# Kernel optimization log

Measured on AMD Instinct MI355X. Metric: run time of the kernel, lower is better.

Reference implementation:

```python
import jax, jax.numpy as jnp
import numpy as np
import math

B, L, H, D, HID = 2, 1024, 16, 64, 1024  # batch, seq, heads, head_dim, hidden_size


def _rope_tables(seq_len, dim):
    inv_freq = 1.0 / (10000.0 ** (jnp.arange(0, dim, 2, dtype=jnp.float32) / dim))
    t = jnp.arange(seq_len, dtype=jnp.float32)
    freqs = jnp.outer(t, inv_freq)            # (L, D/2)
    emb = jnp.concatenate([freqs, freqs], -1)  # (L, D)
    return jnp.cos(emb), jnp.sin(emb)


def _rotate_half(x):
    x1, x2 = jnp.split(x, 2, axis=-1)
    return jnp.concatenate([-x2, x1], axis=-1)


def _apply_rope(x, cos, sin):
    # x: (B,H,L,D); cos/sin: (1,1,L,D)
    return x * cos + _rotate_half(x) * sin


def setup_inputs() -> dict:
    key = jax.random.key(0)
    ks = jax.random.split(key, 8)
    s = 0.02
    return {
        "x": jax.random.normal(ks[0], (B, L, HID), jnp.float32),
        "w_qkv": jax.random.normal(ks[1], (HID, 3 * H * D), jnp.float32) * s,
        "w_o": jax.random.normal(ks[2], (H * D, HID), jnp.float32) * s,
        "log_p": jax.random.normal(ks[3], (H, 1, 1), jnp.float32) * 0.02,
        "log_a": jax.random.normal(ks[4], (H, 1, 1), jnp.float32) * 0.02,
        "w1": jax.random.normal(ks[5], (2 * H, 2 * H), jnp.float32) * s,
        "b1": jnp.zeros((2 * H,), jnp.float32),
        "w2": jax.random.normal(ks[6], (2 * H, H), jnp.float32) * s,
        "b2": jnp.zeros((H,), jnp.float32),
    }


def _forward(x, w_qkv, w_o, log_p, log_a, w1, b1, w2, b2):
    Bx, Lx, _ = x.shape
    qkv = jnp.dot(x, w_qkv).reshape(Bx, Lx, 3, H, D)
    qkv = jnp.transpose(qkv, (2, 0, 3, 1, 4))  # (3,B,H,L,D)
    q, k, v = qkv[0], qkv[1], qkv[2]

    cos, sin = _rope_tables(Lx, D)
    cos, sin = cos[None, None], sin[None, None]
    q = _apply_rope(q, cos, sin)
    k = _apply_rope(k, cos, sin)

    scale = 1.0 / math.sqrt(D)
    scores = jnp.einsum('bhid,bhjd->bhij', q, k) * scale  # (B,H,L,L)

    # Kerple bias: -p * log1p(a * |m-n|), per head
    pos = jnp.arange(Lx, dtype=jnp.float32)
    dist = jnp.abs(pos[None, :] - pos[:, None])            # (L,L)
    p = jax.nn.softplus(log_p)
    a = jax.nn.softplus(log_a)
    kerple = -p * jnp.log1p(a * dist[None])                # (H,L,L)

    # DAPE MLP refinement over head channel
    attn_t = jnp.transpose(scores, (0, 2, 3, 1))           # (B,L,L,H)
    kerple_t = jnp.broadcast_to(jnp.transpose(kerple, (1, 2, 0))[None], attn_t.shape)
    combined = jnp.concatenate([attn_t, kerple_t], axis=-1)  # (B,L,L,2H)
    hdn = jax.nn.gelu(jnp.dot(combined, w1) + b1, approximate=False)
    refined = jnp.dot(hdn, w2) + b2                        # (B,L,L,H)
    refined = jnp.transpose(refined, (0, 3, 1, 2))         # (B,H,L,L)

    scores = scores + kerple[None] + refined

    causal = jnp.tril(jnp.ones((Lx, Lx), dtype=bool))
    scores = jnp.where(causal[None, None], scores, -jnp.inf)
    weights = jax.nn.softmax(scores, axis=-1)
    out = jnp.einsum('bhij,bhjd->bhid', weights, v)        # (B,H,L,D)
    out = jnp.transpose(out, (0, 2, 1, 3)).reshape(Bx, Lx, H * D)
    return jnp.dot(out, w_o)


def reference(x, w_qkv, w_o, log_p, log_a, w1, b1, w2, b2):
    return _forward(x, w_qkv, w_o, log_p, log_a, w1, b1, w2, b2)
```

## Files before the change

kernel.cpp:

```cpp
#include <hip/hip_runtime.h>
#include <math.h>

#define Bv 2
#define Lv 1024
#define Hv 16
#define Dv 64
#define HIDv 1024

typedef unsigned short u16;
typedef short bf16x8 __attribute__((ext_vector_type(8)));
typedef unsigned short u16x4 __attribute__((ext_vector_type(4)));
typedef float f32x4 __attribute__((ext_vector_type(4)));

__device__ __forceinline__ u16 f2b(float f) {
    union { float f; unsigned u; } v; v.f = f;
    return (u16)((v.u + 0x8000u) >> 16);
}
__device__ __forceinline__ float b2f(u16 h) {
    union { unsigned u; float f; } v; v.u = ((unsigned)h) << 16;
    return v.f;
}

__device__ __forceinline__ void gl2lds16(const u16* g, u16* l) {
    __builtin_amdgcn_global_load_lds(
        (const __attribute__((address_space(1))) unsigned int*)g,
        (__attribute__((address_space(3))) unsigned int*)l,
        16, 0, 0);
}

__device__ __forceinline__ float gelu_fast(float x) {
    float x2 = x * x;
    float inner = __builtin_fmaf(0.044715f * x2, x, x);
    float e = __expf(-1.5957691216057308f * inner);
    return x / (1.0f + e);
}

__global__ __launch_bounds__(256) void qkv_rope(
    const u16* __restrict__ A, const u16* __restrict__ B,
    const float* __restrict__ ctab, const float* __restrict__ stab,
    u16* __restrict__ q, u16* __restrict__ k, u16* __restrict__ vT)
{
    __shared__ u16 As[128 * 32];
    __shared__ u16 Bs[128 * 32];
    __shared__ u16 Ct[128 * 136];

    const int m0 = blockIdx.y * 128;
    const int n0 = blockIdx.x * 128;
    const int K = 1024;

    const int tid = threadIdx.x;
    const int lane = tid & 63;
    const int wave = tid >> 6;
    const int wm0 = (wave >> 1) * 64;
    const int wn0 = (wave & 1) * 64;
    const int fr = lane & 15;
    const int fq = lane >> 4;

    f32x4 acc[4][4];
    #pragma unroll
    for (int i = 0; i < 4; ++i)
        #pragma unroll
        for (int j = 0; j < 4; ++j) acc[i][j] = (f32x4){0.f, 0.f, 0.f, 0.f};

    for (int k0 = 0; k0 < K; k0 += 32) {
        #pragma unroll
        for (int it = 0; it < 2; ++it) {
            int cid = tid + it * 256;
            int r = cid >> 2, ch = cid & 3;
            gl2lds16(A + (long long)(m0 + r) * K + k0 + ch * 8, &As[cid * 8]);
        }
        #pragma unroll
        for (int it = 0; it < 2; ++it) {
            int cid = tid + it * 256;
            int r = cid >> 2, ch = cid & 3;
            gl2lds16(B + (long long)(n0 + r) * K + k0 + ch * 8, &Bs[cid * 8]);
        }
        __syncthreads();
        bf16x8 af[4], bfr[4];
        #pragma unroll
        for (int i = 0; i < 4; ++i)
            af[i] = *(const bf16x8*)&As[(wm0 + i * 16 + fr) * 32 + fq * 8];
        #pragma unroll
        for (int j = 0; j < 4; ++j)
            bfr[j] = *(const bf16x8*)&Bs[(wn0 + j * 16 + fr) * 32 + fq * 8];
        #pragma unroll
        for (int i = 0; i < 4; ++i)
            #pragma unroll
            for (int j = 0; j < 4; ++j)
                acc[i][j] = __builtin_amdgcn_mfma_f32_16x16x32_bf16(
                    af[i], bfr[j], acc[i][j], 0, 0, 0);
        __syncthreads();
    }

    const int b = m0 >> 10;

    if (n0 >= 2048) {
        #pragma unroll
        for (int i = 0; i < 4; ++i)
            #pragma unroll
            for (int j = 0; j < 4; ++j) {
                int vcol = (n0 - 2048) + wn0 + j * 16 + fr;
                int head = vcol >> 6, d = vcol & 63;
                int l = ((m0 + wm0 + i * 16 + fq * 4) & 1023);
                u16 o[4];
                #pragma unroll
                for (int r = 0; r < 4; ++r) o[r] = f2b(acc[i][j][r]);
                *(u16x4*)&vT[((long long)(b * 16 + head) * 64 + d) * 1024 + l] =
                    *(u16x4*)o;
            }
        return;
    }

    #pragma unroll
    for (int i = 0; i < 4; ++i)
        #pragma unroll
        for (int j = 0; j < 4; ++j)
            #pragma unroll
            for (int r = 0; r < 4; ++r)
                Ct[(wm0 + i * 16 + fq * 4 + r) * 136 + wn0 + j * 16 + fr] =
                    f2b(acc[i][j][r]);
    __syncthreads();

    u16* dst = (n0 >= 1024) ? k : q;
    const int nh = n0 & 1023;
    #pragma unroll
    for (int c = 0; c < 8; ++c) {
        int cid = tid + c * 256;
        int row = cid >> 4, kc = cid & 15;
        int l = (m0 + row) & 1023;
        int head = (nh >> 6) + (kc >> 3);
        int d0 = (kc & 7) * 8;
        bf16x8 x  = *(const bf16x8*)&Ct[row * 136 + kc * 8];
        bf16x8 xp = *(const bf16x8*)&Ct[row * 136 + (kc ^ 4) * 8];
        float4 c0 = *(const float4*)&ctab[l * 64 + d0];
        float4 c1 = *(const float4*)&ctab[l * 64 + d0 + 4];
        float4 s0 = *(const float4*)&stab[l * 64 + d0];
        float4 s1 = *(const float4*)&stab[l * 64 + d0 + 4];
        float ct[8] = {c0.x, c0.y, c0.z, c0.w, c1.x, c1.y, c1.z, c1.w};
        float st[8] = {s0.x, s0.y, s0.z, s0.w, s1.x, s1.y, s1.z, s1.w};
        u16 o[8];
        #pragma unroll
        for (int e = 0; e < 8; ++e)
            o[e] = f2b(b2f((u16)x[e]) * ct[e] + b2f((u16)xp[e]) * st[e]);
        *(bf16x8*)&dst[((long long)(b * 16 + head) * 1024 + l) * 64 + d0] =
            *(bf16x8*)o;
    }
}

template<int BM, int BN, int WM, int WN, bool CBF16>
__global__ __launch_bounds__(256) void gemm_bt(
    const u16* __restrict__ A, const u16* __restrict__ B, void* __restrict__ Cv,
    int M, int N, int K, float alpha)
{
    constexpr int NW = BN / WN;
    constexpr int MI = WM / 16;
    constexpr int NI = WN / 16;
    constexpr int LDB = BN + 8;
    constexpr int LDF = BN + 4;
    __shared__ u16 As[BM * 32];
    __shared__ u16 Bs[BN * 32];
    __shared__ u16 Ctb[CBF16 ? BM * LDB : 1];
    __shared__ float Ctf[CBF16 ? 1 : BM * LDF];

    const int m0 = blockIdx.y * BM;
    const int n0 = blockIdx.x * BN;

    const int tid = threadIdx.x;
    const int lane = tid & 63;
    const int wave = tid >> 6;
    const int wm0 = (wave / NW) * WM;
    const int wn0 = (wave % NW) * WN;
    const int fr = lane & 15;
    const int fq = lane >> 4;

    f32x4 acc[MI][NI];
    #pragma unroll
    for (int i = 0; i < MI; ++i)
        #pragma unroll
        for (int j = 0; j < NI; ++j) acc[i][j] = (f32x4){0.f, 0.f, 0.f, 0.f};

    for (int k0 = 0; k0 < K; k0 += 32) {
        #pragma unroll
        for (int it = 0; it < BM / 64; ++it) {
            int cid = tid + it * 256;
            int r = cid >> 2, ch = cid & 3;
            gl2lds16(A + (long long)(m0 + r) * K + k0 + ch * 8, &As[cid * 8]);
        }
        #pragma unroll
        for (int it = 0; it < BN / 64; ++it) {
            int cid = tid + it * 256;
            int r = cid >> 2, ch = cid & 3;
            gl2lds16(B + (long long)(n0 + r) * K + k0 + ch * 8, &Bs[cid * 8]);
        }
        __syncthreads();
        bf16x8 af[MI], bfr[NI];
        #pragma unroll
        for (int i = 0; i < MI; ++i)
            af[i] = *(const bf16x8*)&As[(wm0 + i * 16 + fr) * 32 + fq * 8];
        #pragma unroll
        for (int j = 0; j < NI; ++j)
            bfr[j] = *(const bf16x8*)&Bs[(wn0 + j * 16 + fr) * 32 + fq * 8];
        #pragma unroll
        for (int i = 0; i < MI; ++i)
            #pragma unroll
            for (int j = 0; j < NI; ++j)
                acc[i][j] = __builtin_amdgcn_mfma_f32_16x16x32_bf16(
                    af[i], bfr[j], acc[i][j], 0, 0, 0);
        __syncthreads();
    }

    #pragma unroll
    for (int i = 0; i < MI; ++i)
        #pragma unroll
        for (int j = 0; j < NI; ++j)
            #pragma unroll
            for (int r = 0; r < 4; ++r) {
                int row = wm0 + i * 16 + fq * 4 + r;
                int col = wn0 + j * 16 + fr;
                float v = acc[i][j][r] * alpha;
                if (CBF16) Ctb[row * LDB + col] = f2b(v);
                else       Ctf[row * LDF + col] = v;
            }
    __syncthreads();
    if (CBF16) {
        constexpr int CPR = BN / 8;
        #pragma unroll
        for (int c = 0; c < (BM * BN) / (8 * 256); ++c) {
            int cid = tid + c * 256;
            int row = cid / CPR, kc = cid % CPR;
            *(bf16x8*)((u16*)Cv + (long long)(m0 + row) * N + n0 + kc * 8) =
                *(const bf16x8*)&Ctb[row * LDB + kc * 8];
        }
    } else {
        constexpr int CPR = BN / 4;
        #pragma unroll
        for (int c = 0; c < (BM * BN) / (4 * 256); ++c) {
            int cid = tid + c * 256;
            int row = cid / CPR, kc = cid % CPR;
            *(float4*)((float*)Cv + (long long)(m0 + row) * N + n0 + kc * 4) =
                *(const float4*)&Ctf[row * LDF + kc * 4];
        }
    }
}

__global__ __launch_bounds__(256) void qk_direct(
    const u16* __restrict__ Q, const u16* __restrict__ K, u16* __restrict__ S)
{
    const int m0 = blockIdx.y * 128;
    const int n0 = blockIdx.x * 128;
    if (n0 > m0) return;
    const u16* A = Q + (long long)blockIdx.z * 65536;
    const u16* B = K + (long long)blockIdx.z * 65536;
    u16* C = S + (long long)blockIdx.z * 1048576;

    __shared__ u16 Ct[128 * 136];

    const int tid = threadIdx.x;
    const int lane = tid & 63;
    const int wave = tid >> 6;
    const int wm0 = (wave >> 1) * 64;
    const int wn0 = (wave & 1) * 64;
    const int fr = lane & 15;
    const int fq = lane >> 4;

    bf16x8 af[4][2], bfr[4][2];
    #pragma unroll
    for (int i = 0; i < 4; ++i)
        #pragma unroll
        for (int p = 0; p < 2; ++p) {
            af[i][p]  = *(const bf16x8*)&A[(m0 + wm0 + i * 16 + fr) * 64 + p * 32 + fq * 8];
            bfr[i][p] = *(const bf16x8*)&B[(n0 + wn0 + i * 16 + fr) * 64 + p * 32 + fq * 8];
        }

    f32x4 acc[4][4];
    #pragma unroll
    for (int i = 0; i < 4; ++i)
        #pragma unroll
        for (int j = 0; j < 4; ++j) acc[i][j] = (f32x4){0.f, 0.f, 0.f, 0.f};

    #pragma unroll
    for (int p = 0; p < 2; ++p)
        #pragma unroll
        for (int i = 0; i < 4; ++i)
            #pragma unroll
            for (int j = 0; j < 4; ++j)
                acc[i][j] = __builtin_amdgcn_mfma_f32_16x16x32_bf16(
                    af[i][p], bfr[j][p], acc[i][j], 0, 0, 0);

    #pragma unroll
    for (int i = 0; i < 4; ++i)
        #pragma unroll
        for (int j = 0; j < 4; ++j)
            #pragma unroll
            for (int r = 0; r < 4; ++r)
                Ct[(wm0 + i * 16 + fq * 4 + r) * 136 + wn0 + j * 16 + fr] =
                    f2b(acc[i][j][r] * 0.125f);
    __syncthreads();
    #pragma unroll
    for (int c = 0; c < 8; ++c) {
        int cid = tid + c * 256;
        int row = cid >> 4, kc = cid & 15;
        *(bf16x8*)&C[(long long)(m0 + row) * 1024 + n0 + kc * 8] =
            *(const bf16x8*)&Ct[row * 136 + kc * 8];
    }
}

__global__ __launch_bounds__(256) void pv_direct(
    const u16* __restrict__ W, const u16* __restrict__ VT, u16* __restrict__ O)
{
    const int m0 = blockIdx.x * 64;
    const int bh = blockIdx.y;
    const u16* A = W + (long long)bh * 1048576;
    const u16* B = VT + (long long)bh * 65536;
    const int b = bh >> 4, h = bh & 15;

    __shared__ u16 Ct[64 * 72];

    const int tid = threadIdx.x;
    const int lane = tid & 63;
    const int wave = tid >> 6;
    const int wm0 = (wave >> 1) * 32;
    const int wn0 = (wave & 1) * 32;
    const int fr = lane & 15;
    const int fq = lane >> 4;

    f32x4 acc[2][2];
    #pragma unroll
    for (int i = 0; i < 2; ++i)
        #pragma unroll
        for (int j = 0; j < 2; ++j) acc[i][j] = (f32x4){0.f, 0.f, 0.f, 0.f};

    const int Kend = m0 + 64;
    for (int k0 = 0; k0 < Kend; k0 += 64) {
        bf16x8 af[2][2], bfr[2][2];
        #pragma unroll
        for (int p = 0; p < 2; ++p) {
            #pragma unroll
            for (int i = 0; i < 2; ++i)
                af[p][i] = *(const bf16x8*)&A[(m0 + wm0 + i * 16 + fr) * 1024 + k0 + p * 32 + fq * 8];
            #pragma unroll
            for (int j = 0; j < 2; ++j)
                bfr[p][j] = *(const bf16x8*)&B[(wn0 + j * 16 + fr) * 1024 + k0 + p * 32 + fq * 8];
        }
        #pragma unroll
        for (int p = 0; p < 2; ++p)
            #pragma unroll
            for (int i = 0; i < 2; ++i)
                #pragma unroll
                for (int j = 0; j < 2; ++j)
                    acc[i][j] = __builtin_amdgcn_mfma_f32_16x16x32_bf16(
                        af[p][i], bfr[p][j], acc[i][j], 0, 0, 0);
    }

    #pragma unroll
    for (int i = 0; i < 2; ++i)
        #pragma unroll
        for (int j = 0; j < 2; ++j)
            #pragma unroll
            for (int r = 0; r < 4; ++r)
                Ct[(wm0 + i * 16 + fq * 4 + r) * 72 + wn0 + j * 16 + fr] =
                    f2b(acc[i][j][r]);
    __syncthreads();
    const long long ob = (long long)b * 1048576 + h * 64;
    #pragma unroll
    for (int c = 0; c < 2; ++c) {
        int cid = tid + c * 256;
        int row = cid >> 3, kc = cid & 7;
        *(bf16x8*)&O[ob + (long long)(m0 + row) * 1024 + kc * 8] =
            *(const bf16x8*)&Ct[row * 72 + kc * 8];
    }
}

__global__ __launch_bounds__(256) void prep(
    const float* __restrict__ x, u16* __restrict__ x_bf,
    const float* __restrict__ w_qkv, u16* __restrict__ wqkvT,
    const float* __restrict__ w_o, u16* __restrict__ woT,
    const float* __restrict__ log_p, const float* __restrict__ log_a,
    u16* __restrict__ ktab, float* __restrict__ ctab, float* __restrict__ stab)
{
    __shared__ float tile[64][65];
    const int bid = blockIdx.x;
    const int tid = threadIdx.x;

    if (bid < 8192) {
        int i = bid * 256 + tid;
        x_bf[i] = f2b(x[i]);
        return;
    }
    if (bid >= 9280) {
        int idx = (bid - 9280) * 256 + tid;
        int e = idx & 65535;
        int l = e >> 6, d = e & 63;
        float inv_freq = __expf((float)(d & 31) * -0.28782313662425574f);
        float arg = (float)l * inv_freq;
        if (idx < 65536) ctab[e] = __cosf(arg);
        else             stab[e] = (d < 32) ? -__sinf(arg) : __sinf(arg);
        return;
    }
    if (bid >= 9216) {
        int idx = (bid - 9216) * 256 + tid;
        int h = idx & 15, dist = idx >> 4;
        float pp = log1pf(__expf(log_p[h]));
        float aa = log1pf(__expf(log_a[h]));
        ktab[idx] = f2b(-pp * log1pf(aa * (float)dist));
        return;
    }
    const float* src; u16* dst; int M, N, bx, by;
    if (bid < 8960) { int t = bid - 8192; bx = t % 48; by = t / 48; src = w_qkv; dst = wqkvT; M = 1024; N = 3072; }
    else            { int t = bid - 8960; bx = t % 16; by = t / 16; src = w_o;   dst = woT;   M = 1024; N = 1024; }
    const int m0 = by * 64, n0 = bx * 64;
    #pragma unroll
    for (int c = 0; c < 4; ++c) {
        int f = tid + c * 256;
        int r = f >> 4, cs = (f & 15) * 4;
        float4 v = *(const float4*)&src[(long long)(m0 + r) * N + n0 + cs];
        tile[r][cs] = v.x; tile[r][cs + 1] = v.y;
        tile[r][cs + 2] = v.z; tile[r][cs + 3] = v.w;
    }
    __syncthreads();
    int nl = tid >> 2, ms = (tid & 3) * 16;
    u16 outv[16];
    #pragma unroll
    for (int c = 0; c < 16; ++c) outv[c] = f2b(tile[ms + c][nl]);
    *(bf16x8*)&dst[(long long)(n0 + nl) * M + m0 + ms]     = *(bf16x8*)&outv[0];
    *(bf16x8*)&dst[(long long)(n0 + nl) * M + m0 + ms + 8] = *(bf16x8*)&outv[8];
}

#define LSTR 1044

__global__ __launch_bounds__(512) void dape_soft(
    u16* __restrict__ S, const u16* __restrict__ ktab,
    const float* __restrict__ w1, const float* __restrict__ b1,
    const float* __restrict__ w2, const float* __restrict__ b2)
{
    const int i = 1023 - blockIdx.x;
    const int b = blockIdx.y;

    __shared__ u16 logits[16 * LSTR];
    __shared__ u16 comb[256 * 36];

    const int tid = threadIdx.x;
    const int lane = tid & 63;
    const int wave = tid >> 6;
    const int fr = lane & 15;
    const int fq = lane >> 4;

    bf16x8 B1a, B1b, B2f, Bid;
    #pragma unroll
    for (int e = 0; e < 8; ++e) {
        int c = fq * 8 + e;
        B1a[e] = (short)f2b(w1[c * 32 + fr]);
        B1b[e] = (short)f2b(w1[c * 32 + 16 + fr]);
        B2f[e] = (short)f2b(w2[c * 16 + fr]);
        Bid[e] = (short)((c == fr || c == 16 + fr) ? 0x3F80 : 0);
    }
    const float b1a = b1[fr], b1b = b1[16 + fr], b2v = b2[fr];

    const long long sbase = (long long)b * 16 * 1048576 + (long long)i * 1024;
    const int nchunk = (i >> 8) + 1;

    for (int c = 0; c < nchunk; ++c) {
        {
            const int jo = tid & 255;
            const int half = tid >> 8;
            const int j = c * 256 + jo;
            u16 row[8];
            #pragma unroll
            for (int h = 0; h < 8; ++h)
                row[h] = S[sbase + (long long)(half * 8 + h) * 1048576 + j];
            const int dist = (i - j > 0) ? (i - j) : 0;
            *(bf16x8*)&comb[jo * 36 + half * 8] = *(bf16x8*)row;
            *(bf16x8*)&comb[jo * 36 + 16 + half * 8] =
                *(const bf16x8*)&ktab[dist * 16 + half * 8];
        }
        __syncthreads();

        for (int t = wave; t < 16; t += 8) {
            const int jt = c * 256 + t * 16;
            if (jt > i) continue;

            bf16x8 A1 = *(const bf16x8*)&comb[(t * 16 + fr) * 36 + fq * 8];
            f32x4 z = (f32x4){0.f, 0.f, 0.f, 0.f};
            f32x4 ac1a = __builtin_amdgcn_mfma_f32_16x16x32_bf16(A1, B1a, z, 0, 0, 0);
            f32x4 ac1b = __builtin_amdgcn_mfma_f32_16x16x32_bf16(A1, B1b, z, 0, 0, 0);
            f32x4 cres = __builtin_amdgcn_mfma_f32_16x16x32_bf16(
                A1, Bid, (f32x4){b2v, b2v, b2v, b2v}, 0, 0, 0);

            u16* hidp = &comb[t * 16 * 36];
            #pragma unroll
            for (int r = 0; r < 4; ++r) {
                float g0 = gelu_fast(ac1a[r] + b1a);
                float g1 = gelu_fast(ac1b[r] + b1b);
                hidp[(fq * 4 + r) * 36 + fr]      = f2b(g0);
                hidp[(fq * 4 + r) * 36 + 16 + fr] = f2b(g1);
            }
            bf16x8 A2 = *(const bf16x8*)&hidp[fr * 36 + fq * 8];
            f32x4 ac2 = __builtin_amdgcn_mfma_f32_16x16x32_bf16(A2, B2f, cres, 0, 0, 0);

            u16 o[4];
            #pragma unroll
            for (int r = 0; r < 4; ++r) o[r] = f2b(ac2[r]);
            *(u16x4*)&logits[fr * LSTR + jt + fq * 4] = *(u16x4*)o;
        }
        __syncthreads();
    }

    const int we = ((i >> 7) + 1) << 7;
    for (int hh = wave; hh < 16; hh += 8) {
        float vals[16];
        float mx = -3.0e38f;
        #pragma unroll
        for (int s = 0; s < 4; ++s) {
            u16x4 r4 = *(const u16x4*)&logits[hh * LSTR + lane * 4 + 256 * s];
            #pragma unroll
            for (int e = 0; e < 4; ++e) {
                int j = lane * 4 + 256 * s + e;
                float v = (j <= i) ? b2f(r4[e]) : -3.0e38f;
                vals[s * 4 + e] = v;
                mx = fmaxf(mx, v);
            }
        }
        #pragma unroll
        for (int off = 1; off < 64; off <<= 1)
            mx = fmaxf(mx, __shfl_xor(mx, off));
        float sm = 0.f;
        #pragma unroll
        for (int e = 0; e < 16; ++e) {
            float ev = (vals[e] > -1.0e37f) ? __expf(vals[e] - mx) : 0.f;
            vals[e] = ev;
            sm += ev;
        }
        #pragma unroll
        for (int off = 1; off < 64; off <<= 1)
            sm += __shfl_xor(sm, off);
        const float inv = 1.0f / sm;
        const long long hb = sbase + (long long)hh * 1048576;
        #pragma unroll
        for (int s = 0; s < 4; ++s) {
            int j0v = lane * 4 + 256 * s;
            if (j0v < we) {
                u16 o[4];
                #pragma unroll
                for (int e = 0; e < 4; ++e) o[e] = f2b(vals[s * 4 + e] * inv);
                *(u16x4*)&S[hb + j0v] = *(u16x4*)o;
            }
        }
    }
}

extern "C" void kernel_launch(void* const* d_in, const int* in_sizes, int n_in,
                              void* d_out, int out_size, void* d_ws, size_t ws_size,
                              hipStream_t stream)
{
    const float* x     = (const float*)d_in[0];
    const float* w_qkv = (const float*)d_in[1];
    const float* w_o   = (const float*)d_in[2];
    const float* log_p = (const float*)d_in[3];
    const float* log_a = (const float*)d_in[4];
    const float* w1    = (const float*)d_in[5];
    const float* b1    = (const float*)d_in[6];
    const float* w2    = (const float*)d_in[7];
    const float* b2    = (const float*)d_in[8];
    float* out = (float*)d_out;

    char* p = (char*)d_ws;
    u16* x_bf    = (u16*)p;    p += 2097152ll * 2;
    u16* wqkvT   = (u16*)p;    p += 3145728ll * 2;
    u16* woT     = (u16*)p;    p += 1048576ll * 2;
    u16* q_bf    = (u16*)p;    p += 2097152ll * 2;
    u16* k_bf    = (u16*)p;    p += 2097152ll * 2;
    u16* vT      = (u16*)p;    p += 2097152ll * 2;
    u16* scores  = (u16*)p;    p += 33554432ll * 2;
    u16* attn_bf = (u16*)p;    p += 2097152ll * 2;
    u16* ktab    = (u16*)p;    p += 16384ll * 2;
    float* ctab  = (float*)p;  p += 65536ll * 4;
    float* stab  = (float*)p;  p += 65536ll * 4;

    prep<<<9792, 256, 0, stream>>>(x, x_bf, w_qkv, wqkvT, w_o, woT,
                                   log_p, log_a, ktab, ctab, stab);

    qkv_rope<<<dim3(24, 16), 256, 0, stream>>>(
        x_bf, wqkvT, ctab, stab, q_bf, k_bf, vT);

    qk_direct<<<dim3(8, 8, 32), 256, 0, stream>>>(q_bf, k_bf, scores);

    dape_soft<<<dim3(1024, 2), 512, 0, stream>>>(
        scores, ktab, w1, b1, w2, b2);

    pv_direct<<<dim3(16, 32), 256, 0, stream>>>(scores, vT, attn_bf);

    gemm_bt<64, 64, 32, 32, false><<<dim3(16, 32, 1), 256, 0, stream>>>(
        attn_bf, woT, out, 2048, 1024, 1024, 1.0f);
}
```

Before: 221.7 us.

## Shrink QKV tile to 64 rows, alias LDS, skip masked softmax chunks

The QKV+RoPE GEMM now uses 64x128 tiles instead of 128x128, doubling the grid to 768 blocks. The epilogue staging buffer aliases the A/B LDS tiles, which cuts shared memory and raises occupancy on a GPU with many CUs. The softmax in the DAPE kernel skips fully masked 256-column segments and drops the per-element mask test on fully valid segments. Division is replaced with a hardware reciprocal in gelu and the softmax normalisation. Smaller tiles lower per-block data reuse, and the approximate reciprocal changes precision slightly.

```diff
diff --git a/kernel.cpp b/kernel.cpp
--- a/kernel.cpp
+++ b/kernel.cpp
@@ -32,7 +32,7 @@
     float x2 = x * x;
     float inner = __builtin_fmaf(0.044715f * x2, x, x);
     float e = __expf(-1.5957691216057308f * inner);
-    return x / (1.0f + e);
+    return x * __builtin_amdgcn_rcpf(1.0f + e);
 }
 
 __global__ __launch_bounds__(256) void qkv_rope(
@@ -40,34 +40,33 @@
     const float* __restrict__ ctab, const float* __restrict__ stab,
     u16* __restrict__ q, u16* __restrict__ k, u16* __restrict__ vT)
 {
-    __shared__ u16 As[128 * 32];
-    __shared__ u16 Bs[128 * 32];
-    __shared__ u16 Ct[128 * 136];
-
-    const int m0 = blockIdx.y * 128;
+    __shared__ __align__(16) char pool[64 * 136 * 2];
+    u16* As = (u16*)pool;
+    u16* Bs = (u16*)(pool + 8192);
+    u16* Ct = (u16*)pool;
+
+    const int m0 = blockIdx.y * 64;
     const int n0 = blockIdx.x * 128;
     const int K = 1024;
 
     const int tid = threadIdx.x;
     const int lane = tid & 63;
     const int wave = tid >> 6;
-    const int wm0 = (wave >> 1) * 64;
+    const int wm0 = (wave >> 1) * 32;
     const int wn0 = (wave & 1) * 64;
     const int fr = lane & 15;
     const int fq = lane >> 4;
 
-    f32x4 acc[4][4];
-    #pragma unroll
-    for (int i = 0; i < 4; ++i)
+    f32x4 acc[2][4];
+    #pragma unroll
+    for (int i = 0; i < 2; ++i)
         #pragma unroll
         for (int j = 0; j < 4; ++j) acc[i][j] = (f32x4){0.f, 0.f, 0.f, 0.f};
 
     for (int k0 = 0; k0 < K; k0 += 32) {
-        #pragma unroll
-        for (int it = 0; it < 2; ++it) {
-            int cid = tid + it * 256;
-            int r = cid >> 2, ch = cid & 3;
-            gl2lds16(A + (long long)(m0 + r) * K + k0 + ch * 8, &As[cid * 8]);
+        {
+            int r = tid >> 2, ch = tid & 3;
+            gl2lds16(A + (long long)(m0 + r) * K + k0 + ch * 8, &As[tid * 8]);
         }
         #pragma unroll
         for (int it = 0; it < 2; ++it) {
@@ -76,15 +75,15 @@
             gl2lds16(B + (long long)(n0 + r) * K + k0 + ch * 8, &Bs[cid * 8]);
         }
         __syncthreads();
-        bf16x8 af[4], bfr[4];
-        #pragma unroll
-        for (int i = 0; i < 4; ++i)
+        bf16x8 af[2], bfr[4];
+        #pragma unroll
+        for (int i = 0; i < 2; ++i)
             af[i] = *(const bf16x8*)&As[(wm0 + i * 16 + fr) * 32 + fq * 8];
         #pragma unroll
         for (int j = 0; j < 4; ++j)
             bfr[j] = *(const bf16x8*)&Bs[(wn0 + j * 16 + fr) * 32 + fq * 8];
         #pragma unroll
-        for (int i = 0; i < 4; ++i)
+        for (int i = 0; i < 2; ++i)
             #pragma unroll
             for (int j = 0; j < 4; ++j)
                 acc[i][j] = __builtin_amdgcn_mfma_f32_16x16x32_bf16(
@@ -96,7 +95,7 @@
 
     if (n0 >= 2048) {
         #pragma unroll
-        for (int i = 0; i < 4; ++i)
+        for (int i = 0; i < 2; ++i)
             #pragma unroll
             for (int j = 0; j < 4; ++j) {
                 int vcol = (n0 - 2048) + wn0 + j * 16 + fr;
@@ -112,7 +111,7 @@
     }
 
     #pragma unroll
-    for (int i = 0; i < 4; ++i)
+    for (int i = 0; i < 2; ++i)
         #pragma unroll
         for (int j = 0; j < 4; ++j)
             #pragma unroll
@@ -124,7 +123,7 @@
     u16* dst = (n0 >= 1024) ? k : q;
     const int nh = n0 & 1023;
     #pragma unroll
-    for (int c = 0; c < 8; ++c) {
+    for (int c = 0; c < 4; ++c) {
         int cid = tid + c * 256;
         int row = cid >> 4, kc = cid & 15;
         int l = (m0 + row) & 1023;
@@ -458,6 +457,7 @@
 
     const long long sbase = (long long)b * 16 * 1048576 + (long long)i * 1024;
     const int nchunk = (i >> 8) + 1;
+    const int slast = i >> 8;
 
     for (int c = 0; c < nchunk; ++c) {
         {
@@ -511,13 +511,23 @@
         float mx = -3.0e38f;
         #pragma unroll
         for (int s = 0; s < 4; ++s) {
+            if (s > slast) continue;
             u16x4 r4 = *(const u16x4*)&logits[hh * LSTR + lane * 4 + 256 * s];
-            #pragma unroll
-            for (int e = 0; e < 4; ++e) {
-                int j = lane * 4 + 256 * s + e;
-                float v = (j <= i) ? b2f(r4[e]) : -3.0e38f;
-                vals[s * 4 + e] = v;
-                mx = fmaxf(mx, v);
+            if (s < slast) {
+                #pragma unroll
+                for (int e = 0; e < 4; ++e) {
+                    float v = b2f(r4[e]);
+                    vals[s * 4 + e] = v;
+                    mx = fmaxf(mx, v);
+                }
+            } else {
+                #pragma unroll
+                for (int e = 0; e < 4; ++e) {
+                    int j = lane * 4 + 256 * s + e;
+                    float v = (j <= i) ? b2f(r4[e]) : -3.0e38f;
+                    vals[s * 4 + e] = v;
+                    mx = fmaxf(mx, v);
+                }
             }
         }
         #pragma unroll
@@ -525,20 +535,40 @@
             mx = fmaxf(mx, __shfl_xor(mx, off));
         float sm = 0.f;
         #pragma unroll
-        for (int e = 0; e < 16; ++e) {
-            float ev = (vals[e] > -1.0e37f) ? __expf(vals[e] - mx) : 0.f;
-            vals[e] = ev;
-            sm += ev;
+        for (int s = 0; s < 4; ++s) {
+            if (s > slast) continue;
+            if (s < slast) {
+                #pragma unroll
+                for (int e = 0; e < 4; ++e) {
+                    float ev = __expf(vals[s * 4 + e] - mx);
+                    vals[s * 4 + e] = ev;
+                    sm += ev;
+                }
+            } else {
+                #pragma unroll
+                for (int e = 0; e < 4; ++e) {
+                    float ev = (vals[s * 4 + e] > -1.0e37f)
+                                   ? __expf(vals[s * 4 + e] - mx) : 0.f;
+                    vals[s * 4 + e] = ev;
+                    sm += ev;
+                }
+            }
         }
         #pragma unroll
         for (int off = 1; off < 64; off <<= 1)
             sm += __shfl_xor(sm, off);
-        const float inv = 1.0f / sm;
+        const float inv = __builtin_amdgcn_rcpf(sm);
         const long long hb = sbase + (long long)hh * 1048576;
         #pragma unroll
         for (int s = 0; s < 4; ++s) {
+            if (s > slast) continue;
             int j0v = lane * 4 + 256 * s;
-            if (j0v < we) {
+            if (s < slast) {
+                u16 o[4];
+                #pragma unroll
+                for (int e = 0; e < 4; ++e) o[e] = f2b(vals[s * 4 + e] * inv);
+                *(u16x4*)&S[hb + j0v] = *(u16x4*)o;
+            } else if (j0v < we) {
                 u16 o[4];
                 #pragma unroll
                 for (int e = 0; e < 4; ++e) o[e] = f2b(vals[s * 4 + e] * inv);
@@ -579,7 +609,7 @@
     prep<<<9792, 256, 0, stream>>>(x, x_bf, w_qkv, wqkvT, w_o, woT,
                                    log_p, log_a, ktab, ctab, stab);
 
-    qkv_rope<<<dim3(24, 16), 256, 0, stream>>>(
+    qkv_rope<<<dim3(24, 32), 256, 0, stream>>>(
         x_bf, wqkvT, ctab, stab, q_bf, k_bf, vT);
 
     qk_direct<<<dim3(8, 8, 32), 256, 0, stream>>>(q_bf, k_bf, scores);
```

Result: faster. 215.1 us (-3.0%).
